# Kernel optimization log

Measured on AMD Instinct MI355X. Metric: run time of the kernel, lower is better.

The kernel has to match this reference:

```python
import jax, jax.numpy as jnp
import numpy as np

N_NODES = 50000
N_EDGES = 800000
D_IN = 256
D_OUT = 128
EPS = 1e-9


def setup_inputs() -> dict:
    key = jax.random.key(0)
    ks = jax.random.split(key, 6)
    feat = jax.random.normal(ks[0], (N_NODES, D_IN), dtype=jnp.float32)
    edge_row = jax.random.randint(ks[1], (N_EDGES,), 0, N_NODES)
    edge_col = jax.random.randint(ks[2], (N_EDGES,), 0, N_NODES)
    # normalized adjacency values (positive, ~1/degree scale)
    edge_val = jax.random.uniform(ks[3], (N_EDGES,), dtype=jnp.float32) / 16.0
    # xavier_uniform for Linear(dim_in, dim_out) weights, stored as [D_IN, D_OUT]
    limit = float(np.sqrt(6.0 / (D_IN + D_OUT)))
    W0 = jax.random.uniform(ks[4], (D_IN, D_OUT), minval=-limit, maxval=limit, dtype=jnp.float32)
    W1 = jax.random.uniform(ks[5], (D_IN, D_OUT), minval=-limit, maxval=limit, dtype=jnp.float32)
    zeros = jnp.zeros((D_OUT,), dtype=jnp.float32)
    ones = jnp.ones((D_OUT,), dtype=jnp.float32)
    return {
        "feat": feat,
        "W0": W0, "b0": zeros, "scale0": ones, "offset0": zeros,
        "W1": W1, "b1": zeros, "scale1": ones, "offset1": zeros,
        "edge_row": edge_row, "edge_col": edge_col, "edge_val": edge_val,
    }


def _spmm(edge_row, edge_col, edge_val, x):
    # out[r] += val * x[c] for each edge (r, c, val)  -- sparse adj @ x
    msgs = edge_val[:, None] * x[edge_col]  # [E, D]
    return jax.ops.segment_sum(msgs, edge_row, num_segments=N_NODES)


def _feat_trans(x, W, b, scale, offset):
    h = jax.nn.relu(x @ W + b)  # [N, D_OUT]
    mean = jnp.mean(h, axis=1, keepdims=True)
    var = jnp.var(h, axis=1, keepdims=True) + EPS  # unbiased=False (population var)
    return (h - mean) * scale * jax.lax.rsqrt(var) + offset


def reference(feat, W0, b0, scale0, offset0, W1, b1, scale1, offset1,
              edge_row, edge_col, edge_val):
    # non-first-layer path: feat_hop = [X, A @ X] (order=1), dropout p=0 is identity
    hop1 = _spmm(edge_row, edge_col, edge_val, feat)
    f0 = _feat_trans(feat, W0, b0, scale0, offset0)
    f1 = _feat_trans(hop1, W1, b1, scale1, offset1)
    return jnp.concatenate([f0, f1], axis=1)  # aggr == 'concat'
```

## Files before the change

kernel.cpp:

```cpp
#include <hip/hip_runtime.h>

#define N_NODES 50000
#define N_EDGES 800000
#define D_IN    256
#define D_OUT   128
#define EPS     1e-9f
#define PAD     88

#define SCATTER_BLOCKS 196
#define GEMM_MBLKS     391

#define RPB    64
#define NBUCK  782
#define BCAP   1344

typedef __attribute__((ext_vector_type(8))) short bf16x8;
typedef __attribute__((ext_vector_type(4))) float floatx4;

__device__ __forceinline__ ushort f2bf(float x) {
    unsigned u = __float_as_uint(x);
    u += 0x7fffu + ((u >> 16) & 1u);
    return (ushort)(u >> 16);
}

#define WB_BLOCKS  32
__global__ __launch_bounds__(256) void prep_small(
    const float* __restrict__ W0, const float* __restrict__ W1,
    ushort* __restrict__ Wb, int* __restrict__ gcnt)
{
    int bid = blockIdx.x;
    int t   = threadIdx.x;
    if (bid == 0) {
        for (int i = t; i < NBUCK; i += 256) gcnt[i] = 0;
    } else {
        int g  = (bid - 1) * 256 + t;
        int n  = g >> 5;
        int kq = g & 31;
        const float* W = (n < 128) ? W0 : W1;
        int nn = n & 127;
        union { ushort us[8]; uint4 v; } tmp;
#pragma unroll
        for (int j = 0; j < 8; ++j)
            tmp.us[j] = f2bf(W[(size_t)(kq * 8 + j) * D_OUT + nn]);
        *(uint4*)&Wb[(size_t)n * D_IN + kq * 8] = tmp.v;
    }
}

__global__ __launch_bounds__(256, 3) void gemm_scatter(
    const float* __restrict__ feat, const ushort* __restrict__ Wb,
    const float* __restrict__ bias, const float* __restrict__ scale,
    const float* __restrict__ offset,
    float* __restrict__ out, ushort* __restrict__ Y1,
    const int* __restrict__ er, const int* __restrict__ ec,
    const float* __restrict__ ev, int* __restrict__ gcnt,
    uint2* __restrict__ bedge)
{
    __shared__ ushort As[128 * PAD];
    __shared__ ushort Bs[128 * PAD];

    const int t = threadIdx.x;

    if (blockIdx.x < SCATTER_BLOCKS) {
        int* hist = (int*)As;
        int* base = (int*)Bs;
        for (int i = t; i < NBUCK; i += 256) hist[i] = 0;
        __syncthreads();

        int ebase = blockIdx.x * 4096;
        int   bkt[16], rnk[16];
        uint2 pk[16];
#pragma unroll
        for (int u = 0; u < 16; ++u) {
            int e = ebase + u * 256 + t;
            bool ok = (e < N_EDGES);
            int   r = ok ? er[e] : 0;
            int   c = ok ? ec[e] : 0;
            float v = ok ? ev[e] : 0.f;
            bkt[u] = ok ? (r >> 6) : -1;
            pk[u]  = make_uint2(((unsigned)(r & 63) << 16) | (unsigned)c,
                                __float_as_uint(v));
            if (ok) rnk[u] = atomicAdd(&hist[r >> 6], 1);
        }
        __syncthreads();
        for (int i = t; i < NBUCK; i += 256) {
            int h = hist[i];
            base[i] = h ? atomicAdd(&gcnt[i], h) : 0;
        }
        __syncthreads();
#pragma unroll
        for (int u = 0; u < 16; ++u) {
            if (bkt[u] >= 0) {
                int pos = base[bkt[u]] + rnk[u];
                if (pos < BCAP)
                    bedge[(size_t)bkt[u] * BCAP + pos] = pk[u];
            }
        }
        return;
    }

    const int gbid = blockIdx.x - SCATTER_BLOCKS;
    const int half = gbid / GEMM_MBLKS;
    const int mblk = gbid % GEMM_MBLKS;
    const int wave = t >> 6, lane = t & 63;
    const int quad = lane >> 4, l16 = lane & 15;
    const int m0   = mblk * 128;
    const int n0   = half * 128;

    floatx4 acc[2][8];
#pragma unroll
    for (int mt = 0; mt < 2; ++mt)
#pragma unroll
        for (int nt = 0; nt < 8; ++nt)
            acc[mt][nt] = (floatx4){0.f, 0.f, 0.f, 0.f};

    for (int kt = 0; kt < D_IN; kt += 64) {
#pragma unroll
        for (int i = 0; i < 4; ++i) {
            int g = t + i * 256;
            int row = g >> 3, kq = g & 7;
            int grow = m0 + row;
            union { ushort us[8]; uint4 v; } tmp;
            tmp.v = make_uint4(0u, 0u, 0u, 0u);
            if (grow < N_NODES) {
                const float* p = &feat[(size_t)grow * D_IN + kt + kq * 8];
                float4 v0 = *(const float4*)p;
                float4 v1 = *(const float4*)(p + 4);
                tmp.us[0] = f2bf(v0.x); tmp.us[1] = f2bf(v0.y);
                tmp.us[2] = f2bf(v0.z); tmp.us[3] = f2bf(v0.w);
                tmp.us[4] = f2bf(v1.x); tmp.us[5] = f2bf(v1.y);
                tmp.us[6] = f2bf(v1.z); tmp.us[7] = f2bf(v1.w);
            }
            *(uint4*)&As[row * PAD + kq * 8] = tmp.v;
        }
#pragma unroll
        for (int i = 0; i < 4; ++i) {
            int g = t + i * 256;
            int row = g >> 3, kq = g & 7;
            *(uint4*)&Bs[row * PAD + kq * 8] =
                *(const uint4*)&Wb[(size_t)(n0 + row) * D_IN + kt + kq * 8];
        }
        __syncthreads();

#pragma unroll
        for (int kk = 0; kk < 64; kk += 32) {
            bf16x8 a[2], b[8];
#pragma unroll
            for (int mt = 0; mt < 2; ++mt)
                a[mt] = *(bf16x8*)&As[(wave * 32 + mt * 16 + l16) * PAD + kk + quad * 8];
#pragma unroll
            for (int nt = 0; nt < 8; ++nt)
                b[nt] = *(bf16x8*)&Bs[(nt * 16 + l16) * PAD + kk + quad * 8];
#pragma unroll
            for (int mt = 0; mt < 2; ++mt)
#pragma unroll
                for (int nt = 0; nt < 8; ++nt)
                    acc[mt][nt] = __builtin_amdgcn_mfma_f32_16x16x32_bf16(
                        a[mt], b[nt], acc[mt][nt], 0, 0, 0);
        }
        __syncthreads();
    }

    if (half == 0) {
        float bb[8], sc[8], of[8];
#pragma unroll
        for (int nt = 0; nt < 8; ++nt) {
            bb[nt] = bias[nt * 16 + l16];
            sc[nt] = scale[nt * 16 + l16];
            of[nt] = offset[nt * 16 + l16];
        }
#pragma unroll
        for (int mt = 0; mt < 2; ++mt)
#pragma unroll
            for (int i = 0; i < 4; ++i) {
                float h[8], s = 0.f, q = 0.f;
#pragma unroll
                for (int nt = 0; nt < 8; ++nt) {
                    h[nt] = fmaxf(acc[mt][nt][i] + bb[nt], 0.f);
                    s += h[nt];
                    q += h[nt] * h[nt];
                }
#pragma unroll
                for (int m = 1; m < 16; m <<= 1) {
                    s += __shfl_xor(s, m);
                    q += __shfl_xor(q, m);
                }
                float mean = s * (1.f / 128.f);
                float inv  = rsqrtf(q * (1.f / 128.f) - mean * mean + EPS);
                int row = m0 + wave * 32 + mt * 16 + quad * 4 + i;
                if (row < N_NODES) {
#pragma unroll
                    for (int nt = 0; nt < 8; ++nt)
                        out[(size_t)row * 256 + nt * 16 + l16] =
                            (h[nt] - mean) * sc[nt] * inv + of[nt];
                }
            }
    } else {
#pragma unroll
        for (int mt = 0; mt < 2; ++mt)
#pragma unroll
            for (int i = 0; i < 4; ++i) {
                int row = m0 + wave * 32 + mt * 16 + quad * 4 + i;
                if (row < N_NODES) {
#pragma unroll
                    for (int nt = 0; nt < 8; ++nt)
                        Y1[(size_t)row * D_OUT + nt * 16 + l16] =
                            f2bf(acc[mt][nt][i]);
                }
            }
    }
}

__global__ __launch_bounds__(512) void spmm_csr_ln(
    const int* __restrict__ gcnt, const uint2* __restrict__ bedge,
    const ushort* __restrict__ Y,
    const float* __restrict__ bias, const float* __restrict__ scale,
    const float* __restrict__ offset, float* __restrict__ out)
{
    __shared__ ushort lcol[BCAP];
    __shared__ float  lval[BCAP];
    __shared__ int    cnt[RPB];
    __shared__ int    offx[RPB];

    const int t      = threadIdx.x;
    const int bucket = blockIdx.x;
    const int r0     = bucket * RPB;
    const int nrows  = min(RPB, N_NODES - r0);
    int ne = gcnt[bucket];
    ne = ne < BCAP ? ne : BCAP;

    if (t < RPB) cnt[t] = 0;
    __syncthreads();

    const size_t base = (size_t)bucket * BCAP;
    int   erA = -1, erB = -1, erC = -1;
    int   ecA = 0,  ecB = 0,  ecC = 0;
    float evA = 0.f, evB = 0.f, evC = 0.f;
    int   rkA = 0,  rkB = 0,  rkC = 0;
    if (t < ne) {
        uint2 p = bedge[base + t];
        erA = (int)(p.x >> 16); ecA = (int)(p.x & 0xffffu);
        evA = __uint_as_float(p.y);
        rkA = atomicAdd(&cnt[erA], 1);
    }
    if (t + 512 < ne) {
        uint2 p = bedge[base + t + 512];
        erB = (int)(p.x >> 16); ecB = (int)(p.x & 0xffffu);
        evB = __uint_as_float(p.y);
        rkB = atomicAdd(&cnt[erB], 1);
    }
    if (t + 1024 < ne) {
        uint2 p = bedge[base + t + 1024];
        erC = (int)(p.x >> 16); ecC = (int)(p.x & 0xffffu);
        evC = __uint_as_float(p.y);
        rkC = atomicAdd(&cnt[erC], 1);
    }
    __syncthreads();

    if (t < RPB) {
        int c = cnt[t], x = c;
#pragma unroll
        for (int s = 1; s < RPB; s <<= 1) {
            int w = __shfl_up(x, s);
            if (t >= s) x += w;
        }
        offx[t] = x - c;
    }
    __syncthreads();

    if (erA >= 0) { int k = offx[erA] + rkA; lcol[k] = (ushort)ecA; lval[k] = evA; }
    if (erB >= 0) { int k = offx[erB] + rkB; lcol[k] = (ushort)ecB; lval[k] = evB; }
    if (erC >= 0) { int k = offx[erC] + rkC; lcol[k] = (ushort)ecC; lval[k] = evC; }
    __syncthreads();

    const int wave = t >> 6, lane = t & 63;
    const int cidx = lane * 2;
    const float b0v = bias[cidx],   b1v = bias[cidx + 1];
    const float s0v = scale[cidx],  s1v = scale[cidx + 1];
    const float o0v = offset[cidx], o1v = offset[cidx + 1];

    for (int ri = wave; ri < nrows; ri += 8) {
        int beg = offx[ri], n = cnt[ri];
        float ax = 0.f, ay = 0.f;
        int j = 0;
        for (; j + 8 <= n; j += 8) {
            unsigned yv[8]; float vv[8]; int cc[8];
#pragma unroll
            for (int u = 0; u < 8; ++u) {
                cc[u] = lcol[beg + j + u];
                vv[u] = lval[beg + j + u];
                yv[u] = *(const unsigned*)&Y[(size_t)cc[u] * D_OUT + cidx];
            }
#pragma unroll
            for (int u = 0; u < 8; ++u) {
                ax = fmaf(vv[u], __uint_as_float(yv[u] << 16), ax);
                ay = fmaf(vv[u], __uint_as_float(yv[u] & 0xffff0000u), ay);
            }
        }
        for (; j < n; ++j) {
            int   c  = lcol[beg + j];
            float vj = lval[beg + j];
            unsigned yv = *(const unsigned*)&Y[(size_t)c * D_OUT + cidx];
            ax = fmaf(vj, __uint_as_float(yv << 16), ax);
            ay = fmaf(vj, __uint_as_float(yv & 0xffff0000u), ay);
        }
        float h0 = fmaxf(ax + b0v, 0.f);
        float h1 = fmaxf(ay + b1v, 0.f);
        float s = h0 + h1, q = h0 * h0 + h1 * h1;
#pragma unroll
        for (int m = 1; m < 64; m <<= 1) {
            s += __shfl_xor(s, m);
            q += __shfl_xor(q, m);
        }
        float mean = s * (1.f / 128.f);
        float inv  = rsqrtf(q * (1.f / 128.f) - mean * mean + EPS);
        int row = r0 + ri;
        float2 o;
        o.x = (h0 - mean) * s0v * inv + o0v;
        o.y = (h1 - mean) * s1v * inv + o1v;
        *(float2*)&out[(size_t)row * 256 + 128 + cidx] = o;
    }
}

extern "C" void kernel_launch(void* const* d_in, const int* in_sizes, int n_in,
                              void* d_out, int out_size, void* d_ws, size_t ws_size,
                              hipStream_t stream)
{
    const float* feat = (const float*)d_in[0];
    const float* W0   = (const float*)d_in[1];
    const float* b0   = (const float*)d_in[2];
    const float* s0   = (const float*)d_in[3];
    const float* o0   = (const float*)d_in[4];
    const float* W1   = (const float*)d_in[5];
    const float* b1   = (const float*)d_in[6];
    const float* s1   = (const float*)d_in[7];
    const float* o1   = (const float*)d_in[8];
    const int*   er   = (const int*)d_in[9];
    const int*   ec   = (const int*)d_in[10];
    const float* ev   = (const float*)d_in[11];
    float* out = (float*)d_out;

    char*   wsb   = (char*)d_ws;
    ushort* Wb    = (ushort*)(wsb);
    ushort* Y1    = (ushort*)(wsb + 131072);
    int*    gcnt  = (int*)   (wsb + 12931072);
    uint2*  bedge = (uint2*) (wsb + 12935168);

    prep_small<<<1 + WB_BLOCKS, 256, 0, stream>>>(W0, W1, Wb, gcnt);

    gemm_scatter<<<SCATTER_BLOCKS + 2 * GEMM_MBLKS, 256, 0, stream>>>(
        feat, Wb, b0, s0, o0, out, Y1, er, ec, ev, gcnt, bedge);

    spmm_csr_ln<<<NBUCK, 512, 0, stream>>>(
        gcnt, bedge, Y1, b1, s1, o1, out);
}
```

Measured before the change: 179.2 us.

## Load A fragments directly from global into registers, widen GEMM blocks to 512 threads

The GEMM no longer stages the fp32 feature tile through LDS. Each wave now loads its own 16 rows straight from global memory into MFMA A fragments and converts them to bf16 in registers, and only the weight tile is kept in shared memory with a 128-wide K step. Blocks grow to 512 threads with a launch bound of 4, each wave handling 16 rows instead of 32, and the scatter blocks are reshaped to match. This cuts LDS traffic and synchronisation and should allow more occupancy. The cost is that each B fragment is reused across fewer rows, and the direct global loads are strided per lane rather than fully coalesced.

```diff
diff --git a/kernel.cpp b/kernel.cpp
--- a/kernel.cpp
+++ b/kernel.cpp
@@ -5,7 +5,7 @@
 #define D_IN    256
 #define D_OUT   128
 #define EPS     1e-9f
-#define PAD     88
+#define BPAD    136
 
 #define SCATTER_BLOCKS 196
 #define GEMM_MBLKS     391
@@ -21,6 +21,15 @@
     unsigned u = __float_as_uint(x);
     u += 0x7fffu + ((u >> 16) & 1u);
     return (ushort)(u >> 16);
+}
+
+__device__ __forceinline__ bf16x8 packbf(float4 a, float4 b) {
+    union { ushort us[8]; bf16x8 v; } r;
+    r.us[0] = f2bf(a.x); r.us[1] = f2bf(a.y);
+    r.us[2] = f2bf(a.z); r.us[3] = f2bf(a.w);
+    r.us[4] = f2bf(b.x); r.us[5] = f2bf(b.y);
+    r.us[6] = f2bf(b.z); r.us[7] = f2bf(b.w);
+    return r.v;
 }
 
 #define WB_BLOCKS  32
@@ -46,7 +55,7 @@
     }
 }
 
-__global__ __launch_bounds__(256, 3) void gemm_scatter(
+__global__ __launch_bounds__(512, 4) void gemm_scatter(
     const float* __restrict__ feat, const ushort* __restrict__ Wb,
     const float* __restrict__ bias, const float* __restrict__ scale,
     const float* __restrict__ offset,
@@ -55,23 +64,22 @@
     const float* __restrict__ ev, int* __restrict__ gcnt,
     uint2* __restrict__ bedge)
 {
-    __shared__ ushort As[128 * PAD];
-    __shared__ ushort Bs[128 * PAD];
+    __shared__ __align__(16) ushort Bs[128 * BPAD];
 
     const int t = threadIdx.x;
 
     if (blockIdx.x < SCATTER_BLOCKS) {
-        int* hist = (int*)As;
-        int* base = (int*)Bs;
-        for (int i = t; i < NBUCK; i += 256) hist[i] = 0;
+        int* hist = (int*)Bs;
+        int* base = hist + NBUCK;
+        for (int i = t; i < NBUCK; i += 512) hist[i] = 0;
         __syncthreads();
 
         int ebase = blockIdx.x * 4096;
-        int   bkt[16], rnk[16];
-        uint2 pk[16];
-#pragma unroll
-        for (int u = 0; u < 16; ++u) {
-            int e = ebase + u * 256 + t;
+        int   bkt[8], rnk[8];
+        uint2 pk[8];
+#pragma unroll
+        for (int u = 0; u < 8; ++u) {
+            int e = ebase + u * 512 + t;
             bool ok = (e < N_EDGES);
             int   r = ok ? er[e] : 0;
             int   c = ok ? ec[e] : 0;
@@ -82,13 +90,13 @@
             if (ok) rnk[u] = atomicAdd(&hist[r >> 6], 1);
         }
         __syncthreads();
-        for (int i = t; i < NBUCK; i += 256) {
+        for (int i = t; i < NBUCK; i += 512) {
             int h = hist[i];
             base[i] = h ? atomicAdd(&gcnt[i], h) : 0;
         }
         __syncthreads();
 #pragma unroll
-        for (int u = 0; u < 16; ++u) {
+        for (int u = 0; u < 8; ++u) {
             if (bkt[u] >= 0) {
                 int pos = base[bkt[u]] + rnk[u];
                 if (pos < BCAP)
@@ -106,56 +114,45 @@
     const int m0   = mblk * 128;
     const int n0   = half * 128;
 
-    floatx4 acc[2][8];
-#pragma unroll
-    for (int mt = 0; mt < 2; ++mt)
-#pragma unroll
-        for (int nt = 0; nt < 8; ++nt)
-            acc[mt][nt] = (floatx4){0.f, 0.f, 0.f, 0.f};
-
-    for (int kt = 0; kt < D_IN; kt += 64) {
-#pragma unroll
-        for (int i = 0; i < 4; ++i) {
-            int g = t + i * 256;
-            int row = g >> 3, kq = g & 7;
-            int grow = m0 + row;
-            union { ushort us[8]; uint4 v; } tmp;
-            tmp.v = make_uint4(0u, 0u, 0u, 0u);
-            if (grow < N_NODES) {
-                const float* p = &feat[(size_t)grow * D_IN + kt + kq * 8];
-                float4 v0 = *(const float4*)p;
-                float4 v1 = *(const float4*)(p + 4);
-                tmp.us[0] = f2bf(v0.x); tmp.us[1] = f2bf(v0.y);
-                tmp.us[2] = f2bf(v0.z); tmp.us[3] = f2bf(v0.w);
-                tmp.us[4] = f2bf(v1.x); tmp.us[5] = f2bf(v1.y);
-                tmp.us[6] = f2bf(v1.z); tmp.us[7] = f2bf(v1.w);
-            }
-            *(uint4*)&As[row * PAD + kq * 8] = tmp.v;
-        }
-#pragma unroll
-        for (int i = 0; i < 4; ++i) {
-            int g = t + i * 256;
-            int row = g >> 3, kq = g & 7;
-            *(uint4*)&Bs[row * PAD + kq * 8] =
+    const int grow = m0 + wave * 16 + l16;
+    const int arow = grow < N_NODES ? grow : 0;
+    const float* aptr = &feat[(size_t)arow * D_IN + quad * 8];
+
+    floatx4 acc[8];
+#pragma unroll
+    for (int nt = 0; nt < 8; ++nt)
+        acc[nt] = (floatx4){0.f, 0.f, 0.f, 0.f};
+
+    for (int kt = 0; kt < D_IN; kt += 128) {
+#pragma unroll
+        for (int i = 0; i < 8; ++i) {
+            int g = t + i * 512;
+            int row = g >> 4, kq = g & 15;
+            *(uint4*)&Bs[row * BPAD + kq * 8] =
                 *(const uint4*)&Wb[(size_t)(n0 + row) * D_IN + kt + kq * 8];
         }
         __syncthreads();
 
-#pragma unroll
-        for (int kk = 0; kk < 64; kk += 32) {
-            bf16x8 a[2], b[8];
-#pragma unroll
-            for (int mt = 0; mt < 2; ++mt)
-                a[mt] = *(bf16x8*)&As[(wave * 32 + mt * 16 + l16) * PAD + kk + quad * 8];
+        const float* p = aptr + kt;
+        float4 q0 = *(const float4*)(p +  0), q1 = *(const float4*)(p +  4);
+        float4 q2 = *(const float4*)(p + 32), q3 = *(const float4*)(p + 36);
+        float4 q4 = *(const float4*)(p + 64), q5 = *(const float4*)(p + 68);
+        float4 q6 = *(const float4*)(p + 96), q7 = *(const float4*)(p + 100);
+        bf16x8 a0 = packbf(q0, q1), a1 = packbf(q2, q3);
+        bf16x8 a2 = packbf(q4, q5), a3 = packbf(q6, q7);
+
+#pragma unroll
+        for (int s = 0; s < 4; ++s) {
+            bf16x8 a = (s == 0) ? a0 : (s == 1) ? a1 : (s == 2) ? a2 : a3;
+            const int kk = s * 32;
+            bf16x8 b[8];
 #pragma unroll
             for (int nt = 0; nt < 8; ++nt)
-                b[nt] = *(bf16x8*)&Bs[(nt * 16 + l16) * PAD + kk + quad * 8];
-#pragma unroll
-            for (int mt = 0; mt < 2; ++mt)
-#pragma unroll
-                for (int nt = 0; nt < 8; ++nt)
-                    acc[mt][nt] = __builtin_amdgcn_mfma_f32_16x16x32_bf16(
-                        a[mt], b[nt], acc[mt][nt], 0, 0, 0);
+                b[nt] = *(bf16x8*)&Bs[(nt * 16 + l16) * BPAD + kk + quad * 8];
+#pragma unroll
+            for (int nt = 0; nt < 8; ++nt)
+                acc[nt] = __builtin_amdgcn_mfma_f32_16x16x32_bf16(
+                    a, b[nt], acc[nt], 0, 0, 0);
         }
         __syncthreads();
     }
@@ -169,44 +166,40 @@
             of[nt] = offset[nt * 16 + l16];
         }
 #pragma unroll
-        for (int mt = 0; mt < 2; ++mt)
-#pragma unroll
-            for (int i = 0; i < 4; ++i) {
-                float h[8], s = 0.f, q = 0.f;
-#pragma unroll
-                for (int nt = 0; nt < 8; ++nt) {
-                    h[nt] = fmaxf(acc[mt][nt][i] + bb[nt], 0.f);
-                    s += h[nt];
-                    q += h[nt] * h[nt];
-                }
-#pragma unroll
-                for (int m = 1; m < 16; m <<= 1) {
-                    s += __shfl_xor(s, m);
-                    q += __shfl_xor(q, m);
-                }
-                float mean = s * (1.f / 128.f);
-                float inv  = rsqrtf(q * (1.f / 128.f) - mean * mean + EPS);
-                int row = m0 + wave * 32 + mt * 16 + quad * 4 + i;
-                if (row < N_NODES) {
-#pragma unroll
-                    for (int nt = 0; nt < 8; ++nt)
-                        out[(size_t)row * 256 + nt * 16 + l16] =
-                            (h[nt] - mean) * sc[nt] * inv + of[nt];
-                }
-            }
+        for (int i = 0; i < 4; ++i) {
+            float h[8], s = 0.f, q = 0.f;
+#pragma unroll
+            for (int nt = 0; nt < 8; ++nt) {
+                h[nt] = fmaxf(acc[nt][i] + bb[nt], 0.f);
+                s += h[nt];
+                q += h[nt] * h[nt];
+            }
+#pragma unroll
+            for (int m = 1; m < 16; m <<= 1) {
+                s += __shfl_xor(s, m);
+                q += __shfl_xor(q, m);
+            }
+            float mean = s * (1.f / 128.f);
+            float inv  = rsqrtf(q * (1.f / 128.f) - mean * mean + EPS);
+            int row = m0 + wave * 16 + quad * 4 + i;
+            if (row < N_NODES) {
+#pragma unroll
+                for (int nt = 0; nt < 8; ++nt)
+                    out[(size_t)row * 256 + nt * 16 + l16] =
+                        (h[nt] - mean) * sc[nt] * inv + of[nt];
+            }
+        }
     } else {
 #pragma unroll
-        for (int mt = 0; mt < 2; ++mt)
-#pragma unroll
-            for (int i = 0; i < 4; ++i) {
-                int row = m0 + wave * 32 + mt * 16 + quad * 4 + i;
-                if (row < N_NODES) {
-#pragma unroll
-                    for (int nt = 0; nt < 8; ++nt)
-                        Y1[(size_t)row * D_OUT + nt * 16 + l16] =
-                            f2bf(acc[mt][nt][i]);
-                }
-            }
+        for (int i = 0; i < 4; ++i) {
+            int row = m0 + wave * 16 + quad * 4 + i;
+            if (row < N_NODES) {
+#pragma unroll
+                for (int nt = 0; nt < 8; ++nt)
+                    Y1[(size_t)row * D_OUT + nt * 16 + l16] =
+                        f2bf(acc[nt][i]);
+            }
+        }
     }
 }
 
@@ -347,7 +340,7 @@
 
     prep_small<<<1 + WB_BLOCKS, 256, 0, stream>>>(W0, W1, Wb, gcnt);
 
-    gemm_scatter<<<SCATTER_BLOCKS + 2 * GEMM_MBLKS, 256, 0, stream>>>(
+    gemm_scatter<<<SCATTER_BLOCKS + 2 * GEMM_MBLKS, 512, 0, stream>>>(
         feat, Wb, b0, s0, o0, out, Y1, er, ec, ev, gcnt, bedge);
 
     spmm_csr_ln<<<NBUCK, 512, 0, stream>>>(
```

Result: faster. 175.4 us (-2.1%).
